# Optimization experiments

Hardware: AMD Instinct MI355X
Metric: run time of the kernel (lower is better)

Reference implementation:

```python
import jax, jax.numpy as jnp
import numpy as np

B, N, DM, S = 128, 1024, 64, 2
D_IN = 1 + 1 + 2 + DM  # x(1) + m(1) + u(2) + h(DM)


def setup_inputs() -> dict:
    key = jax.random.key(0)
    ks = jax.random.split(key, 12)
    return {
        "x": jax.random.normal(ks[0], (B, 1, N), jnp.float32),
        "m": jax.random.uniform(ks[1], (B, 1, N), jnp.float32),
        "u": jax.random.normal(ks[2], (B, 2, N), jnp.float32),
        "h": jax.random.normal(ks[3], (B, DM, N), jnp.float32),
        # stack of support_len row-normalized-ish adjacencies [S, N, N]
        "adj": jax.random.uniform(ks[4], (S, N, N), jnp.float32) / N,
        "W_in": jax.random.normal(ks[5], (DM, D_IN), jnp.float32) * 0.05,
        "b_in": jnp.zeros((DM,), jnp.float32),
        "W_gc": jax.random.normal(ks[6], (DM, S * DM), jnp.float32) * 0.05,
        "b_gc": jnp.zeros((DM,), jnp.float32),
        "W_out": jax.random.normal(ks[7], (DM, 2 * DM), jnp.float32) * 0.05,
        "b_out": jnp.zeros((DM,), jnp.float32),
        "W_read": jax.random.normal(ks[8], (1, 2 * DM), jnp.float32) * 0.05,
        "b_read": jnp.zeros((1,), jnp.float32),
        "prelu_w": jnp.full((1,), 0.25, jnp.float32),
    }


def _conv1x1(x, W, b):
    # Conv1d(kernel_size=1): [b,c,n] x [o,c] -> [b,o,n]
    return jnp.einsum('bcn,oc->bon', x, W) + b[None, :, None]


def reference(x, m, u, h, adj, W_in, b_in, W_gc, b_gc, W_out, b_out, W_read, b_read, prelu_w):
    # concat inputs on channel dim, then 1x1 conv to d_model
    x_in = jnp.concatenate([x, m, u, h], axis=1)            # [b, d_in, n]
    x_in = _conv1x1(x_in, W_in, b_in)                        # [b, dm, n]
    # SpatialConvOrderK (order=1, include_self=False):
    # per-support aggregation einsum('ncvl,wv->ncwl') with l==1
    agg = jnp.einsum('bcv,swv->bscw', x_in, adj)             # [b, S, dm, n]
    b_, s_, c_, n_ = agg.shape
    agg = agg.reshape(b_, s_ * c_, n_)                       # support-major concat
    gc = _conv1x1(agg, W_gc, b_gc)                           # [b, dm, n]
    out = jnp.concatenate([gc, h], axis=1)                   # [b, 2dm, n]
    out = _conv1x1(out, W_out, b_out)
    out = jnp.where(out >= 0, out, prelu_w[0] * out)         # PReLU (1 param)
    out = jnp.concatenate([out, h], axis=1)                  # [b, 2dm, n]
    return _conv1x1(out, W_read, b_read), out
```

## Files before the change

kernel.cpp:

```cpp
#include <hip/hip_runtime.h>
#include <hip/hip_bf16.h>
#include <stdint.h>

#define NB 128
#define NN 1024
#define NDM 64

typedef __bf16 bf16;
typedef __bf16 bf16x8_t __attribute__((ext_vector_type(8)));
typedef __bf16 bf16x4_t __attribute__((ext_vector_type(4)));
typedef __bf16 bf16x2_t __attribute__((ext_vector_type(2)));
typedef float f32x4 __attribute__((ext_vector_type(4)));

__global__ __launch_bounds__(256) void k_prep_w(
    const float* __restrict__ W_in, const float* __restrict__ b_in,
    const float* __restrict__ W_gc, const float* __restrict__ b_gc,
    const float* __restrict__ W_out, const float* __restrict__ b_out,
    const float* __restrict__ W_read,
    bf16* __restrict__ WAT, float* __restrict__ WYX, float* __restrict__ BIAS,
    bf16* __restrict__ W1B) {
  int i = blockIdx.x * 256 + threadIdx.x;
  if (i < 13312) {
    int r = i >> 6, cc = i & 63;
    int cq = cc >> 3, j = cc & 7;
    int c = ((cq ^ (r & 7)) << 3) + j;
    float val;
    if (r < 128) {
      int s = r >> 6, o = r & 63;
      val = 0.f;
      for (int k = 0; k < 64; ++k) val += W_gc[o * 128 + s * 64 + k] * W_in[k * 68 + 4 + c];
    } else if (r < 192) {
      val = W_out[(r - 128) * 128 + 64 + c];
    } else if (r == 192) {
      val = W_read[64 + c];
    } else {
      val = 0.f;
    }
    WAT[i] = (bf16)val;
  } else if (i < 13824) {
    int idx = i - 13312;
    int r = idx >> 2, j = idx & 3;
    int s = r >> 6, o = r & 63;
    float val = 0.f;
    for (int k = 0; k < 64; ++k) val += W_gc[o * 128 + s * 64 + k] * W_in[k * 68 + j];
    WYX[idx] = val;
  } else if (i < 14032) {
    int r = i - 13824;
    float val = 0.f;
    if (r < 128) {
      int s = r >> 6, o = r & 63;
      for (int k = 0; k < 64; ++k) val += W_gc[o * 128 + s * 64 + k] * b_in[k];
    } else if (r < 192) {
      int o = r - 128;
      val = b_out[o];
      for (int k = 0; k < 64; ++k) val += W_out[o * 128 + k] * b_gc[k];
    }
    BIAS[r] = val;
  } else if (i < 18128) {
    int j = i - 14032;
    int o = j >> 6, c = j & 63;
    W1B[j] = (bf16)W_out[o * 128 + c];
  }
}

__global__ __launch_bounds__(256) void k_adj_bf16(
    const float* __restrict__ adj, bf16* __restrict__ adjb) {
  int i = blockIdx.x * 256 + threadIdx.x;
  float4 v = reinterpret_cast<const float4*>(adj)[i];
  bf16x4_t r;
  r.x = (bf16)v.x; r.y = (bf16)v.y; r.z = (bf16)v.z; r.w = (bf16)v.w;
  reinterpret_cast<bf16x4_t*>(adjb)[i] = r;
}

__global__ __launch_bounds__(256) void k_ht(
    const float* __restrict__ h, bf16* __restrict__ HT, float* __restrict__ out2) {
  __shared__ __align__(16) float T[64 * 128];
  const int t = threadIdx.x;
  const int vb = blockIdx.x * 128;
  const int b = blockIdx.y;
  for (int i = t; i < 2048; i += 256) {
    int r = i >> 5, ck = i & 31;
    float4 v4 = *reinterpret_cast<const float4*>(&h[(size_t)(b * 64 + r) * NN + vb + ck * 4]);
    *reinterpret_cast<float4*>(&T[r * 128 + ck * 4]) = v4;
    *reinterpret_cast<float4*>(&out2[(size_t)(b * 128 + 64 + r) * NN + vb + ck * 4]) = v4;
  }
  __syncthreads();
  const int v = t >> 1, half = t & 1;
#pragma unroll
  for (int cc = 0; cc < 4; ++cc) {
    int cq = half * 4 + cc;
    int cbase = (cq ^ (v & 7)) << 3;
    bf16x8_t pk;
#pragma unroll
    for (int j = 0; j < 8; ++j) pk[j] = (bf16)T[(cbase + j) * 128 + v];
    *reinterpret_cast<bf16x8_t*>(&HT[((size_t)b * NN + vb + v) * 64 + cq * 8]) = pk;
  }
}

__global__ __launch_bounds__(256) void k_build_y(
    const float* __restrict__ x, const float* __restrict__ m, const float* __restrict__ u,
    const bf16* __restrict__ HT, const bf16* __restrict__ WAT,
    const float* __restrict__ WYX, const float* __restrict__ BIAS,
    bf16* __restrict__ Y, float* __restrict__ out2, float* __restrict__ hread) {
  __shared__ __align__(16) bf16 HTs[128 * 64];
  __shared__ __align__(16) bf16 WAs[208 * 64];
  __shared__ __align__(16) float X4L[128 * 4];
  __shared__ __align__(16) float WYXs[128 * 4];
  __shared__ __align__(16) float biasL[208];
  const int t = threadIdx.x;
  const int vb = blockIdx.x * 128;
  const int b = blockIdx.y;

  {
    const bf16* src = HT + ((size_t)b * NN + vb) * 64;
    for (int i = t; i < 1024; i += 256)
      __builtin_amdgcn_global_load_lds((const uint32_t*)(src + i * 8), (uint32_t*)&HTs[i * 8], 16, 0, 0);
    for (int i = t; i < 1664; i += 256)
      __builtin_amdgcn_global_load_lds((const uint32_t*)(WAT + i * 8), (uint32_t*)&WAs[i * 8], 16, 0, 0);
    if (t < 128)
      __builtin_amdgcn_global_load_lds((const uint32_t*)(WYX + t * 4), (uint32_t*)&WYXs[t * 4], 16, 0, 0);
    if (t < 52)
      __builtin_amdgcn_global_load_lds((const uint32_t*)(BIAS + t * 4), (uint32_t*)&biasL[t * 4], 16, 0, 0);
    if (t < 128) {
      int v = t;
      float4 x4;
      x4.x = x[(size_t)b * NN + vb + v];
      x4.y = m[(size_t)b * NN + vb + v];
      x4.z = u[(size_t)(b * 2) * NN + vb + v];
      x4.w = u[(size_t)(b * 2 + 1) * NN + vb + v];
      *reinterpret_cast<float4*>(&X4L[v * 4]) = x4;
    }
  }
  __syncthreads();

  const int wave = t >> 6, lane = t & 63;
  const int q = lane >> 4, lx = lane & 7, o16 = lane & 15;

#pragma unroll
  for (int vi = 0; vi < 2; ++vi) {
    const int vt = wave + vi * 4;
    const int vrow = vt * 16 + o16;
    bf16x8_t af0 = *reinterpret_cast<const bf16x8_t*>(&HTs[vrow * 64 + ((q ^ lx) << 3)]);
    bf16x8_t af1 = *reinterpret_cast<const bf16x8_t*>(&HTs[vrow * 64 + (((q + 4) ^ lx) << 3)]);
    float4 x4r[4];
#pragma unroll
    for (int r = 0; r < 4; ++r)
      x4r[r] = *reinterpret_cast<const float4*>(&X4L[(vt * 16 + q * 4 + r) * 4]);
    const int vg = vb + vt * 16 + q * 4;
    for (int nt = 0; nt < 13; ++nt) {
      const int rr = nt * 16 + o16;
      bf16x8_t bf0 = *reinterpret_cast<const bf16x8_t*>(&WAs[rr * 64 + ((q ^ lx) << 3)]);
      bf16x8_t bf1 = *reinterpret_cast<const bf16x8_t*>(&WAs[rr * 64 + (((q + 4) ^ lx) << 3)]);
      float bsv = biasL[rr];
      f32x4 c0 = {bsv, bsv, bsv, bsv};
      if (nt < 8) {
        float4 wy = *reinterpret_cast<const float4*>(&WYXs[rr * 4]);
#pragma unroll
        for (int r = 0; r < 4; ++r)
          c0[r] += wy.x * x4r[r].x + wy.y * x4r[r].y + wy.z * x4r[r].z + wy.w * x4r[r].w;
      }
      f32x4 acc = __builtin_amdgcn_mfma_f32_16x16x32_bf16(af0, bf0, c0, 0, 0, 0);
      acc = __builtin_amdgcn_mfma_f32_16x16x32_bf16(af1, bf1, acc, 0, 0, 0);
      if (nt < 8) {
        const int s = nt >> 2;
        const int o = rr - s * 64;
        bf16x4_t pk;
        pk.x = (bf16)acc[0]; pk.y = (bf16)acc[1]; pk.z = (bf16)acc[2]; pk.w = (bf16)acc[3];
        *reinterpret_cast<bf16x4_t*>(&Y[(size_t)(b * 64 + o) * 2048 + s * 1024 + vg]) = pk;
      } else if (nt < 12) {
        const int o = rr - 128;
        float4 st; st.x = acc[0]; st.y = acc[1]; st.z = acc[2]; st.w = acc[3];
        *reinterpret_cast<float4*>(&out2[(size_t)(b * 128 + o) * NN + vg]) = st;
      } else if (o16 == 0) {
        float4 st; st.x = acc[0]; st.y = acc[1]; st.z = acc[2]; st.w = acc[3];
        *reinterpret_cast<float4*>(&hread[(size_t)b * NN + vg]) = st;
      }
    }
  }
}

__global__ __launch_bounds__(256) void k_gemm(
    const bf16* __restrict__ Y, const bf16* __restrict__ ADJB,
    const bf16* __restrict__ W1B, const float* __restrict__ W_read,
    const float* __restrict__ b_read, const float* __restrict__ prelu_w,
    const float* __restrict__ hread, float* __restrict__ out0, float* __restrict__ out2) {
  __shared__ __align__(16) union SMem {
    struct { bf16 As[128 * 64]; bf16 Bs[128 * 64]; } st;
    bf16 gcs[2 * 128 * 72];
  } sm;
  __shared__ __align__(16) bf16 W1s[64 * 72];
  __shared__ float Wrs[64];

  const int t = threadIdx.x;
  const int wave = t >> 6, lane = t & 63;
  const int rowA = blockIdx.x * 128;
  const int colB = blockIdx.y * 128;
  const int wm = (wave & 1) * 64, wn = (wave >> 1) * 64;
  const int fr = lane & 15;
  const int q  = lane >> 4;

  for (int i = t; i < 4096; i += 256) W1s[(i >> 6) * 72 + (i & 63)] = W1B[i];
  if (t < 64) Wrs[t] = W_read[t];
  const float pw = prelu_w[0];
  const float br = b_read[0];

  f32x4 acc[4][4];
  const f32x4 zero = {0.f, 0.f, 0.f, 0.f};
#pragma unroll
  for (int i = 0; i < 4; ++i)
#pragma unroll
    for (int j = 0; j < 4; ++j) acc[i][j] = zero;

  int srow[4], sq[4];
#pragma unroll
  for (int j = 0; j < 4; ++j) {
    int c = t + 256 * j;
    srow[j] = c >> 3;
    sq[j] = (c & 7) ^ (srow[j] & 7);
  }
  __syncthreads();

  for (int k0 = 0; k0 < 2048; k0 += 64) {
    const int s = k0 >> 10, v0 = k0 & 1023;
    const bf16* bbase = ADJB + (size_t)s * (1024 * 1024) + v0;
#pragma unroll
    for (int j = 0; j < 4; ++j) {
      int c = t + 256 * j;
      __builtin_amdgcn_global_load_lds(
          (const uint32_t*)(Y + (size_t)(rowA + srow[j]) * 2048 + k0 + sq[j] * 8),
          (uint32_t*)&sm.st.As[c * 8], 16, 0, 0);
    }
#pragma unroll
    for (int j = 0; j < 4; ++j) {
      int c = t + 256 * j;
      __builtin_amdgcn_global_load_lds(
          (const uint32_t*)(bbase + (size_t)(colB + srow[j]) * 1024 + sq[j] * 8),
          (uint32_t*)&sm.st.Bs[c * 8], 16, 0, 0);
    }
    __syncthreads();
#pragma unroll
    for (int k2 = 0; k2 < 64; k2 += 32) {
      bf16x8_t af[4], bfr[4];
#pragma unroll
      for (int i = 0; i < 4; ++i) {
        const int r = wm + i * 16 + fr;
        af[i] = *reinterpret_cast<const bf16x8_t*>(
            &sm.st.As[r * 64 + ((((k2 >> 3) + q) ^ (r & 7)) << 3)]);
      }
#pragma unroll
      for (int i = 0; i < 4; ++i) {
        const int r = wn + i * 16 + fr;
        bfr[i] = *reinterpret_cast<const bf16x8_t*>(
            &sm.st.Bs[r * 64 + ((((k2 >> 3) + q) ^ (r & 7)) << 3)]);
      }
#pragma unroll
      for (int i = 0; i < 4; ++i)
#pragma unroll
        for (int j = 0; j < 4; ++j)
          acc[i][j] = __builtin_amdgcn_mfma_f32_16x16x32_bf16(af[i], bfr[j], acc[i][j], 0, 0, 0);
    }
    __syncthreads();
  }

  {
    const int b2w = wm >> 6;
#pragma unroll
    for (int i = 0; i < 4; ++i) {
      const int cc0 = i * 16 + (lane >> 4) * 4;
#pragma unroll
      for (int j = 0; j < 4; ++j) {
        const int wl = wn + j * 16 + (lane & 15);
        bf16x4_t r;
        r.x = (bf16)acc[i][j][0]; r.y = (bf16)acc[i][j][1];
        r.z = (bf16)acc[i][j][2]; r.w = (bf16)acc[i][j][3];
        *reinterpret_cast<bf16x4_t*>(&sm.gcs[b2w * 9216 + wl * 72 + cc0]) = r;
      }
    }
  }
  __syncthreads();

  const int b2 = wave >> 1, jh = wave & 1;
  const int b = blockIdx.x * 2 + b2;
  const int fk = q * 8;

  f32x4 acc2[4][4];
#pragma unroll
  for (int i = 0; i < 4; ++i)
#pragma unroll
    for (int j = 0; j < 4; ++j) acc2[i][j] = zero;

#pragma unroll
  for (int k2 = 0; k2 < 64; k2 += 32) {
    bf16x8_t af2[4], bf2[4];
#pragma unroll
    for (int i = 0; i < 4; ++i)
      af2[i] = *reinterpret_cast<const bf16x8_t*>(&W1s[(i * 16 + fr) * 72 + k2 + fk]);
#pragma unroll
    for (int j = 0; j < 4; ++j)
      bf2[j] = *reinterpret_cast<const bf16x8_t*>(&sm.gcs[b2 * 9216 + (jh * 64 + j * 16 + fr) * 72 + k2 + fk]);
#pragma unroll
    for (int i = 0; i < 4; ++i)
#pragma unroll
      for (int j = 0; j < 4; ++j)
        acc2[i][j] = __builtin_amdgcn_mfma_f32_16x16x32_bf16(af2[i], bf2[j], acc2[i][j], 0, 0, 0);
  }

  float rd[4] = {0.f, 0.f, 0.f, 0.f};
#pragma unroll
  for (int i = 0; i < 4; ++i) {
    const int ob = i * 16 + (lane >> 4) * 4;
#pragma unroll
    for (int r = 0; r < 4; ++r) {
      const int o = ob + r;
      const float wr = Wrs[o];
#pragma unroll
      for (int j = 0; j < 4; ++j) {
        const int wg = colB + jh * 64 + j * 16 + (lane & 15);
        float* p = &out2[(size_t)(b * 128 + o) * 1024 + wg];
        float val = acc2[i][j][r] + *p;
        val = val >= 0.f ? val : pw * val;
        *p = val;
        rd[j] += wr * val;
      }
    }
  }
#pragma unroll
  for (int j = 0; j < 4; ++j) {
    rd[j] += __shfl_xor(rd[j], 16, 64);
    rd[j] += __shfl_xor(rd[j], 32, 64);
  }
  if (lane < 16) {
#pragma unroll
    for (int j = 0; j < 4; ++j) {
      const int wg = colB + jh * 64 + j * 16 + lane;
      out0[(size_t)b * 1024 + wg] = rd[j] + hread[(size_t)b * 1024 + wg] + br;
    }
  }
}

extern "C" void kernel_launch(void* const* d_in, const int* in_sizes, int n_in,
                              void* d_out, int out_size, void* d_ws, size_t ws_size,
                              hipStream_t stream) {
  (void)in_sizes; (void)n_in; (void)out_size; (void)ws_size;
  const float* x       = (const float*)d_in[0];
  const float* m       = (const float*)d_in[1];
  const float* u       = (const float*)d_in[2];
  const float* h       = (const float*)d_in[3];
  const float* adj     = (const float*)d_in[4];
  const float* W_in    = (const float*)d_in[5];
  const float* b_in    = (const float*)d_in[6];
  const float* W_gc    = (const float*)d_in[7];
  const float* b_gc    = (const float*)d_in[8];
  const float* W_out   = (const float*)d_in[9];
  const float* b_out   = (const float*)d_in[10];
  const float* W_read  = (const float*)d_in[11];
  const float* b_read  = (const float*)d_in[12];
  const float* prelu_w = (const float*)d_in[13];

  char* ws = (char*)d_ws;
  bf16*  Y     = (bf16*)(ws);
  bf16*  ADJB  = (bf16*)(ws + 33554432);
  bf16*  HT    = (bf16*)(ws + 37748736);
  float* HREAD = (float*)(ws + 54525952);
  bf16*  WAT   = (bf16*)(ws + 55050240);
  float* WYX   = (float*)(ws + 55076864);
  float* BIAS  = (float*)(ws + 55078912);
  bf16*  W1B   = (bf16*)(ws + 55079936);

  float* out0 = (float*)d_out;
  float* out2 = out0 + 131072;

  hipLaunchKernelGGL(k_prep_w,  dim3(71),        dim3(256), 0, stream,
                     W_in, b_in, W_gc, b_gc, W_out, b_out, W_read, WAT, WYX, BIAS, W1B);
  hipLaunchKernelGGL(k_adj_bf16,dim3(2048),      dim3(256), 0, stream, adj, ADJB);
  hipLaunchKernelGGL(k_ht,      dim3(8, 128),    dim3(256), 0, stream, h, HT, out2);
  hipLaunchKernelGGL(k_build_y, dim3(8, 128),    dim3(256), 0, stream,
                     x, m, u, HT, WAT, WYX, BIAS, Y, out2, HREAD);
  hipLaunchKernelGGL(k_gemm,    dim3(64, 8),     dim3(256), 0, stream,
                     Y, ADJB, W1B, W_read, b_read, prelu_w, HREAD, out0, out2);
}
```

Before: 201.0 us.

## Fuse prep kernels and move h-projection epilogue into GEMM

Merges the adjacency bf16 conversion with weight prep, and fuses the h transpose into the Y-building kernel so h is read once via direct-to-LDS loads. The W_out·h and W_read·h terms are no longer precomputed into out2/hread; the GEMM epilogue computes them with extra MFMAs reading HT. This removes a full fp32 write and read-modify-write of the out2 first half plus the hread buffer, in exchange for more epilogue MFMA work and uncached HT global loads in the GEMM.

Result: faster. 183.9 us (-8.5%).

```diff
diff --git a/kernel.cpp b/kernel.cpp
--- a/kernel.cpp
+++ b/kernel.cpp
@@ -9,186 +9,172 @@
 typedef __bf16 bf16;
 typedef __bf16 bf16x8_t __attribute__((ext_vector_type(8)));
 typedef __bf16 bf16x4_t __attribute__((ext_vector_type(4)));
-typedef __bf16 bf16x2_t __attribute__((ext_vector_type(2)));
 typedef float f32x4 __attribute__((ext_vector_type(4)));
 
-__global__ __launch_bounds__(256) void k_prep_w(
+__global__ __launch_bounds__(256) void k_prep(
+    const float* __restrict__ adj,
     const float* __restrict__ W_in, const float* __restrict__ b_in,
     const float* __restrict__ W_gc, const float* __restrict__ b_gc,
     const float* __restrict__ W_out, const float* __restrict__ b_out,
     const float* __restrict__ W_read,
-    bf16* __restrict__ WAT, float* __restrict__ WYX, float* __restrict__ BIAS,
-    bf16* __restrict__ W1B) {
-  int i = blockIdx.x * 256 + threadIdx.x;
-  if (i < 13312) {
+    bf16* __restrict__ adjb, bf16* __restrict__ WAT, float* __restrict__ WYX,
+    float* __restrict__ BIAS, bf16* __restrict__ W1B, bf16* __restrict__ A2B,
+    float* __restrict__ HBv) {
+  const int bx = blockIdx.x;
+  if (bx < 2048) {
+    int i = bx * 256 + threadIdx.x;
+    float4 v = reinterpret_cast<const float4*>(adj)[i];
+    bf16x4_t r;
+    r.x = (bf16)v.x; r.y = (bf16)v.y; r.z = (bf16)v.z; r.w = (bf16)v.w;
+    reinterpret_cast<bf16x4_t*>(adjb)[i] = r;
+    return;
+  }
+  int i = (bx - 2048) * 256 + threadIdx.x;
+  if (i < 8192) {
     int r = i >> 6, cc = i & 63;
     int cq = cc >> 3, j = cc & 7;
     int c = ((cq ^ (r & 7)) << 3) + j;
-    float val;
-    if (r < 128) {
-      int s = r >> 6, o = r & 63;
-      val = 0.f;
-      for (int k = 0; k < 64; ++k) val += W_gc[o * 128 + s * 64 + k] * W_in[k * 68 + 4 + c];
-    } else if (r < 192) {
-      val = W_out[(r - 128) * 128 + 64 + c];
-    } else if (r == 192) {
-      val = W_read[64 + c];
-    } else {
-      val = 0.f;
-    }
-    WAT[i] = (bf16)val;
-  } else if (i < 13824) {
-    int idx = i - 13312;
-    int r = idx >> 2, j = idx & 3;
     int s = r >> 6, o = r & 63;
     float val = 0.f;
-    for (int k = 0; k < 64; ++k) val += W_gc[o * 128 + s * 64 + k] * W_in[k * 68 + j];
+    for (int k = 0; k < 64; ++k) val += W_gc[o * 128 + s * 64 + k] * W_in[k * 68 + 4 + c];
+    WAT[i] = (bf16)val;
+  } else if (i < 8704) {
+    int idx = i - 8192;
+    int r = idx >> 2, jj = idx & 3;
+    int s = r >> 6, o = r & 63;
+    float val = 0.f;
+    for (int k = 0; k < 64; ++k) val += W_gc[o * 128 + s * 64 + k] * W_in[k * 68 + jj];
     WYX[idx] = val;
-  } else if (i < 14032) {
-    int r = i - 13824;
+  } else if (i < 8832) {
+    int r = i - 8704;
+    int s = r >> 6, o = r & 63;
     float val = 0.f;
-    if (r < 128) {
-      int s = r >> 6, o = r & 63;
-      for (int k = 0; k < 64; ++k) val += W_gc[o * 128 + s * 64 + k] * b_in[k];
-    } else if (r < 192) {
-      int o = r - 128;
-      val = b_out[o];
-      for (int k = 0; k < 64; ++k) val += W_out[o * 128 + k] * b_gc[k];
-    }
+    for (int k = 0; k < 64; ++k) val += W_gc[o * 128 + s * 64 + k] * b_in[k];
     BIAS[r] = val;
-  } else if (i < 18128) {
-    int j = i - 14032;
+  } else if (i < 12928) {
+    int j = i - 8832;
     int o = j >> 6, c = j & 63;
     W1B[j] = (bf16)W_out[o * 128 + c];
+  } else if (i < 18048) {
+    int j = i - 12928;
+    int r = j >> 6, c = j & 63;
+    float val = 0.f;
+    if (r < 64) val = W_out[r * 128 + 64 + c];
+    else if (r == 64) val = W_read[64 + c];
+    A2B[j] = (bf16)val;
+  } else if (i < 18112) {
+    int o = i - 18048;
+    float val = b_out[o];
+    for (int c = 0; c < 64; ++c) val += W_out[o * 128 + c] * b_gc[c];
+    HBv[o] = val;
   }
 }
 
-__global__ __launch_bounds__(256) void k_adj_bf16(
-    const float* __restrict__ adj, bf16* __restrict__ adjb) {
-  int i = blockIdx.x * 256 + threadIdx.x;
-  float4 v = reinterpret_cast<const float4*>(adj)[i];
-  bf16x4_t r;
-  r.x = (bf16)v.x; r.y = (bf16)v.y; r.z = (bf16)v.z; r.w = (bf16)v.w;
-  reinterpret_cast<bf16x4_t*>(adjb)[i] = r;
-}
-
-__global__ __launch_bounds__(256) void k_ht(
-    const float* __restrict__ h, bf16* __restrict__ HT, float* __restrict__ out2) {
+__global__ __launch_bounds__(256) void k_build(
+    const float* __restrict__ x, const float* __restrict__ m, const float* __restrict__ u,
+    const float* __restrict__ h, const bf16* __restrict__ WAT,
+    const float* __restrict__ WYX, const float* __restrict__ BIAS,
+    bf16* __restrict__ Y, bf16* __restrict__ HT, float* __restrict__ out2) {
   __shared__ __align__(16) float T[64 * 128];
+  __shared__ __align__(16) bf16 HTs[128 * 64];
+  __shared__ __align__(16) bf16 WAs[128 * 64];
+  __shared__ __align__(16) float X4L[128 * 4];
+  __shared__ __align__(16) float WYXs[128 * 4];
+  __shared__ __align__(16) float biasL[128];
   const int t = threadIdx.x;
   const int vb = blockIdx.x * 128;
   const int b = blockIdx.y;
+
+  for (int i = t; i < 2048; i += 256)
+    __builtin_amdgcn_global_load_lds(
+        (const uint32_t*)(h + (size_t)(b * 64 + (i >> 5)) * NN + vb + (i & 31) * 4),
+        (uint32_t*)&T[i * 4], 16, 0, 0);
+  for (int i = t; i < 1024; i += 256)
+    __builtin_amdgcn_global_load_lds((const uint32_t*)(WAT + i * 8), (uint32_t*)&WAs[i * 8], 16, 0, 0);
+  if (t < 128)
+    __builtin_amdgcn_global_load_lds((const uint32_t*)(WYX + t * 4), (uint32_t*)&WYXs[t * 4], 16, 0, 0);
+  if (t < 32)
+    __builtin_amdgcn_global_load_lds((const uint32_t*)(BIAS + t * 4), (uint32_t*)&biasL[t * 4], 16, 0, 0);
+  if (t < 128) {
+    float4 x4;
+    x4.x = x[(size_t)b * NN + vb + t];
+    x4.y = m[(size_t)b * NN + vb + t];
+    x4.z = u[(size_t)(b * 2) * NN + vb + t];
+    x4.w = u[(size_t)(b * 2 + 1) * NN + vb + t];
+    *reinterpret_cast<float4*>(&X4L[t * 4]) = x4;
+  }
+  __syncthreads();
+
+  {
+    const int v = t >> 1, half = t & 1;
+#pragma unroll
+    for (int cc = 0; cc < 4; ++cc) {
+      int cq = half * 4 + cc;
+      int cbase = (cq ^ (v & 7)) << 3;
+      bf16x8_t pk;
+#pragma unroll
+      for (int j = 0; j < 8; ++j) pk[j] = (bf16)T[(cbase + j) * 128 + v];
+      *reinterpret_cast<bf16x8_t*>(&HTs[v * 64 + cq * 8]) = pk;
+      *reinterpret_cast<bf16x8_t*>(&HT[((size_t)(b << 10) + vb + v) * 64 + cq * 8]) = pk;
+    }
+  }
   for (int i = t; i < 2048; i += 256) {
     int r = i >> 5, ck = i & 31;
-    float4 v4 = *reinterpret_cast<const float4*>(&h[(size_t)(b * 64 + r) * NN + vb + ck * 4]);
-    *reinterpret_cast<float4*>(&T[r * 128 + ck * 4]) = v4;
-    *reinterpret_cast<float4*>(&out2[(size_t)(b * 128 + 64 + r) * NN + vb + ck * 4]) = v4;
-  }
-  __syncthreads();
-  const int v = t >> 1, half = t & 1;
-#pragma unroll
-  for (int cc = 0; cc < 4; ++cc) {
-    int cq = half * 4 + cc;
-    int cbase = (cq ^ (v & 7)) << 3;
-    bf16x8_t pk;
-#pragma unroll
-    for (int j = 0; j < 8; ++j) pk[j] = (bf16)T[(cbase + j) * 128 + v];
-    *reinterpret_cast<bf16x8_t*>(&HT[((size_t)b * NN + vb + v) * 64 + cq * 8]) = pk;
-  }
-}
-
-__global__ __launch_bounds__(256) void k_build_y(
-    const float* __restrict__ x, const float* __restrict__ m, const float* __restrict__ u,
-    const bf16* __restrict__ HT, const bf16* __restrict__ WAT,
-    const float* __restrict__ WYX, const float* __restrict__ BIAS,
-    bf16* __restrict__ Y, float* __restrict__ out2, float* __restrict__ hread) {
-  __shared__ __align__(16) bf16 HTs[128 * 64];
-  __shared__ __align__(16) bf16 WAs[208 * 64];
-  __shared__ __align__(16) float X4L[128 * 4];
-  __shared__ __align__(16) float WYXs[128 * 4];
-  __shared__ __align__(16) float biasL[208];
-  const int t = threadIdx.x;
-  const int vb = blockIdx.x * 128;
-  const int b = blockIdx.y;
-
-  {
-    const bf16* src = HT + ((size_t)b * NN + vb) * 64;
-    for (int i = t; i < 1024; i += 256)
-      __builtin_amdgcn_global_load_lds((const uint32_t*)(src + i * 8), (uint32_t*)&HTs[i * 8], 16, 0, 0);
-    for (int i = t; i < 1664; i += 256)
-      __builtin_amdgcn_global_load_lds((const uint32_t*)(WAT + i * 8), (uint32_t*)&WAs[i * 8], 16, 0, 0);
-    if (t < 128)
-      __builtin_amdgcn_global_load_lds((const uint32_t*)(WYX + t * 4), (uint32_t*)&WYXs[t * 4], 16, 0, 0);
-    if (t < 52)
-      __builtin_amdgcn_global_load_lds((const uint32_t*)(BIAS + t * 4), (uint32_t*)&biasL[t * 4], 16, 0, 0);
-    if (t < 128) {
-      int v = t;
-      float4 x4;
-      x4.x = x[(size_t)b * NN + vb + v];
-      x4.y = m[(size_t)b * NN + vb + v];
-      x4.z = u[(size_t)(b * 2) * NN + vb + v];
-      x4.w = u[(size_t)(b * 2 + 1) * NN + vb + v];
-      *reinterpret_cast<float4*>(&X4L[v * 4]) = x4;
-    }
+    float4 hv = *reinterpret_cast<const float4*>(&T[r * 128 + ck * 4]);
+    *reinterpret_cast<float4*>(&out2[(size_t)(b * 128 + 64 + r) * NN + vb + ck * 4]) = hv;
   }
   __syncthreads();
 
   const int wave = t >> 6, lane = t & 63;
   const int q = lane >> 4, lx = lane & 7, o16 = lane & 15;
+  const int offK0 = (q ^ lx) << 3, offK1 = ((q + 4) ^ lx) << 3;
 
 #pragma unroll
   for (int vi = 0; vi < 2; ++vi) {
     const int vt = wave + vi * 4;
     const int vrow = vt * 16 + o16;
-    bf16x8_t af0 = *reinterpret_cast<const bf16x8_t*>(&HTs[vrow * 64 + ((q ^ lx) << 3)]);
-    bf16x8_t af1 = *reinterpret_cast<const bf16x8_t*>(&HTs[vrow * 64 + (((q + 4) ^ lx) << 3)]);
+    bf16x8_t af0 = *reinterpret_cast<const bf16x8_t*>(&HTs[vrow * 64 + offK0]);
+    bf16x8_t af1 = *reinterpret_cast<const bf16x8_t*>(&HTs[vrow * 64 + offK1]);
     float4 x4r[4];
 #pragma unroll
     for (int r = 0; r < 4; ++r)
       x4r[r] = *reinterpret_cast<const float4*>(&X4L[(vt * 16 + q * 4 + r) * 4]);
     const int vg = vb + vt * 16 + q * 4;
-    for (int nt = 0; nt < 13; ++nt) {
+    for (int nt = 0; nt < 8; ++nt) {
       const int rr = nt * 16 + o16;
-      bf16x8_t bf0 = *reinterpret_cast<const bf16x8_t*>(&WAs[rr * 64 + ((q ^ lx) << 3)]);
-      bf16x8_t bf1 = *reinterpret_cast<const bf16x8_t*>(&WAs[rr * 64 + (((q + 4) ^ lx) << 3)]);
+      bf16x8_t bf0 = *reinterpret_cast<const bf16x8_t*>(&WAs[rr * 64 + offK0]);
+      bf16x8_t bf1 = *reinterpret_cast<const bf16x8_t*>(&WAs[rr * 64 + offK1]);
       float bsv = biasL[rr];
-      f32x4 c0 = {bsv, bsv, bsv, bsv};
-      if (nt < 8) {
-        float4 wy = *reinterpret_cast<const float4*>(&WYXs[rr * 4]);
-#pragma unroll
-        for (int r = 0; r < 4; ++r)
-          c0[r] += wy.x * x4r[r].x + wy.y * x4r[r].y + wy.z * x4r[r].z + wy.w * x4r[r].w;
-      }
+      float4 wy = *reinterpret_cast<const float4*>(&WYXs[rr * 4]);
+      f32x4 c0;
+#pragma unroll
+      for (int r = 0; r < 4; ++r)
+        c0[r] = bsv + wy.x * x4r[r].x + wy.y * x4r[r].y + wy.z * x4r[r].z + wy.w * x4r[r].w;
       f32x4 acc = __builtin_amdgcn_mfma_f32_16x16x32_bf16(af0, bf0, c0, 0, 0, 0);
       acc = __builtin_amdgcn_mfma_f32_16x16x32_bf16(af1, bf1, acc, 0, 0, 0);
-      if (nt < 8) {
-        const int s = nt >> 2;
-        const int o = rr - s * 64;
-        bf16x4_t pk;
-        pk.x = (bf16)acc[0]; pk.y = (bf16)acc[1]; pk.z = (bf16)acc[2]; pk.w = (bf16)acc[3];
-        *reinterpret_cast<bf16x4_t*>(&Y[(size_t)(b * 64 + o) * 2048 + s * 1024 + vg]) = pk;
-      } else if (nt < 12) {
-        const int o = rr - 128;
-        float4 st; st.x = acc[0]; st.y = acc[1]; st.z = acc[2]; st.w = acc[3];
-        *reinterpret_cast<float4*>(&out2[(size_t)(b * 128 + o) * NN + vg]) = st;
-      } else if (o16 == 0) {
-        float4 st; st.x = acc[0]; st.y = acc[1]; st.z = acc[2]; st.w = acc[3];
-        *reinterpret_cast<float4*>(&hread[(size_t)b * NN + vg]) = st;
-      }
+      const int s = nt >> 2;
+      const int o = rr - s * 64;
+      bf16x4_t pk;
+      pk.x = (bf16)acc[0]; pk.y = (bf16)acc[1]; pk.z = (bf16)acc[2]; pk.w = (bf16)acc[3];
+      *reinterpret_cast<bf16x4_t*>(&Y[(size_t)(b * 64 + o) * 2048 + s * 1024 + vg]) = pk;
     }
   }
 }
 
 __global__ __launch_bounds__(256) void k_gemm(
     const bf16* __restrict__ Y, const bf16* __restrict__ ADJB,
-    const bf16* __restrict__ W1B, const float* __restrict__ W_read,
+    const bf16* __restrict__ HT,
+    const bf16* __restrict__ W1B, const bf16* __restrict__ A2B,
+    const float* __restrict__ HBv, const float* __restrict__ W_read,
     const float* __restrict__ b_read, const float* __restrict__ prelu_w,
-    const float* __restrict__ hread, float* __restrict__ out0, float* __restrict__ out2) {
+    float* __restrict__ out0, float* __restrict__ out2) {
   __shared__ __align__(16) union SMem {
     struct { bf16 As[128 * 64]; bf16 Bs[128 * 64]; } st;
     bf16 gcs[2 * 128 * 72];
   } sm;
   __shared__ __align__(16) bf16 W1s[64 * 72];
+  __shared__ __align__(16) bf16 A2s[80 * 72];
+  __shared__ float HBs[64];
   __shared__ float Wrs[64];
 
   const int t = threadIdx.x;
@@ -197,10 +183,12 @@
   const int colB = blockIdx.y * 128;
   const int wm = (wave & 1) * 64, wn = (wave >> 1) * 64;
   const int fr = lane & 15;
-  const int q  = lane >> 4;
+  const int q = lane >> 4, lx = lane & 7;
+  const int offK0 = (q ^ lx) << 3, offK1 = ((q + 4) ^ lx) << 3;
 
   for (int i = t; i < 4096; i += 256) W1s[(i >> 6) * 72 + (i & 63)] = W1B[i];
-  if (t < 64) Wrs[t] = W_read[t];
+  for (int i = t; i < 5120; i += 256) A2s[(i >> 6) * 72 + (i & 63)] = A2B[i];
+  if (t < 64) { HBs[t] = HBv[t]; Wrs[t] = W_read[t]; }
   const float pw = prelu_w[0];
   const float br = b_read[0];
 
@@ -211,65 +199,71 @@
 #pragma unroll
     for (int j = 0; j < 4; ++j) acc[i][j] = zero;
 
-  int srow[4], sq[4];
+  const bf16* aSrc[4]; const bf16* bSrc[4];
+  uint32_t* aDst[4]; uint32_t* bDst[4];
 #pragma unroll
   for (int j = 0; j < 4; ++j) {
     int c = t + 256 * j;
-    srow[j] = c >> 3;
-    sq[j] = (c & 7) ^ (srow[j] & 7);
+    int row = c >> 3;
+    int qs = (c & 7) ^ (row & 7);
+    aSrc[j] = Y + (size_t)(rowA + row) * 2048 + qs * 8;
+    bSrc[j] = ADJB + (size_t)(colB + row) * 1024 + qs * 8;
+    aDst[j] = (uint32_t*)&sm.st.As[c * 8];
+    bDst[j] = (uint32_t*)&sm.st.Bs[c * 8];
+  }
+  int rAb[4], rBb[4];
+#pragma unroll
+  for (int i = 0; i < 4; ++i) {
+    rAb[i] = (wm + i * 16 + fr) * 64;
+    rBb[i] = (wn + i * 16 + fr) * 64;
   }
   __syncthreads();
 
-  for (int k0 = 0; k0 < 2048; k0 += 64) {
-    const int s = k0 >> 10, v0 = k0 & 1023;
-    const bf16* bbase = ADJB + (size_t)s * (1024 * 1024) + v0;
-#pragma unroll
-    for (int j = 0; j < 4; ++j) {
-      int c = t + 256 * j;
-      __builtin_amdgcn_global_load_lds(
-          (const uint32_t*)(Y + (size_t)(rowA + srow[j]) * 2048 + k0 + sq[j] * 8),
-          (uint32_t*)&sm.st.As[c * 8], 16, 0, 0);
-    }
-#pragma unroll
-    for (int j = 0; j < 4; ++j) {
-      int c = t + 256 * j;
-      __builtin_amdgcn_global_load_lds(
-          (const uint32_t*)(bbase + (size_t)(colB + srow[j]) * 1024 + sq[j] * 8),
-          (uint32_t*)&sm.st.Bs[c * 8], 16, 0, 0);
-    }
-    __syncthreads();
-#pragma unroll
-    for (int k2 = 0; k2 < 64; k2 += 32) {
-      bf16x8_t af[4], bfr[4];
-#pragma unroll
-      for (int i = 0; i < 4; ++i) {
-        const int r = wm + i * 16 + fr;
-        af[i] = *reinterpret_cast<const bf16x8_t*>(
-            &sm.st.As[r * 64 + ((((k2 >> 3) + q) ^ (r & 7)) << 3)]);
-      }
-#pragma unroll
-      for (int i = 0; i < 4; ++i) {
-        const int r = wn + i * 16 + fr;
-        bfr[i] = *reinterpret_cast<const bf16x8_t*>(
-            &sm.st.Bs[r * 64 + ((((k2 >> 3) + q) ^ (r & 7)) << 3)]);
-      }
-#pragma unroll
-      for (int i = 0; i < 4; ++i)
-#pragma unroll
-        for (int j = 0; j < 4; ++j)
-          acc[i][j] = __builtin_amdgcn_mfma_f32_16x16x32_bf16(af[i], bfr[j], acc[i][j], 0, 0, 0);
-    }
-    __syncthreads();
+  for (int s = 0; s < 2; ++s) {
+    for (int kk = 0; kk < 1024; kk += 64) {
+#pragma unroll
+      for (int j = 0; j < 4; ++j) {
+        __builtin_amdgcn_global_load_lds((const uint32_t*)aSrc[j], aDst[j], 16, 0, 0);
+        aSrc[j] += 64;
+      }
+#pragma unroll
+      for (int j = 0; j < 4; ++j) {
+        __builtin_amdgcn_global_load_lds((const uint32_t*)bSrc[j], bDst[j], 16, 0, 0);
+        bSrc[j] += 64;
+      }
+      __syncthreads();
+#pragma unroll
+      for (int k2 = 0; k2 < 2; ++k2) {
+        const int off = k2 ? offK1 : offK0;
+        bf16x8_t af[4], bfr[4];
+#pragma unroll
+        for (int i = 0; i < 4; ++i)
+          af[i] = *reinterpret_cast<const bf16x8_t*>(&sm.st.As[rAb[i] + off]);
+#pragma unroll
+        for (int i = 0; i < 4; ++i)
+          bfr[i] = *reinterpret_cast<const bf16x8_t*>(&sm.st.Bs[rBb[i] + off]);
+#pragma unroll
+        for (int i = 0; i < 4; ++i)
+#pragma unroll
+          for (int j = 0; j < 4; ++j)
+            acc[i][j] = __builtin_amdgcn_mfma_f32_16x16x32_bf16(af[i], bfr[j], acc[i][j], 0, 0, 0);
+      }
+      __syncthreads();
+    }
+    if (s == 0) {
+#pragma unroll
+      for (int j = 0; j < 4; ++j) bSrc[j] += (1024 * 1024 - 1024);
+    }
   }
 
   {
     const int b2w = wm >> 6;
 #pragma unroll
     for (int i = 0; i < 4; ++i) {
-      const int cc0 = i * 16 + (lane >> 4) * 4;
+      const int cc0 = i * 16 + q * 4;
 #pragma unroll
       for (int j = 0; j < 4; ++j) {
-        const int wl = wn + j * 16 + (lane & 15);
+        const int wl = wn + j * 16 + fr;
         bf16x4_t r;
         r.x = (bf16)acc[i][j][0]; r.y = (bf16)acc[i][j][1];
         r.z = (bf16)acc[i][j][2]; r.w = (bf16)acc[i][j][3];
@@ -281,23 +275,31 @@
 
   const int b2 = wave >> 1, jh = wave & 1;
   const int b = blockIdx.x * 2 + b2;
-  const int fk = q * 8;
-
-  f32x4 acc2[4][4];
-#pragma unroll
-  for (int i = 0; i < 4; ++i)
-#pragma unroll
-    for (int j = 0; j < 4; ++j) acc2[i][j] = zero;
+
+  f32x4 acc2[5][4];
+#pragma unroll
+  for (int i = 0; i < 5; ++i)
+#pragma unroll
+    for (int j = 0; j < 4; ++j) {
+      if (i < 4) {
+        f32x4 c0;
+#pragma unroll
+        for (int r = 0; r < 4; ++r) c0[r] = HBs[i * 16 + q * 4 + r];
+        acc2[i][j] = c0;
+      } else {
+        acc2[i][j] = zero;
+      }
+    }
 
 #pragma unroll
   for (int k2 = 0; k2 < 64; k2 += 32) {
     bf16x8_t af2[4], bf2[4];
 #pragma unroll
     for (int i = 0; i < 4; ++i)
-      af2[i] = *reinterpret_cast<const bf16x8_t*>(&W1s[(i * 16 + fr) * 72 + k2 + fk]);
+      af2[i] = *reinterpret_cast<const bf16x8_t*>(&W1s[(i * 16 + fr) * 72 + k2 + q * 8]);
 #pragma unroll
     for (int j = 0; j < 4; ++j)
-      bf2[j] = *reinterpret_cast<const bf16x8_t*>(&sm.gcs[b2 * 9216 + (jh * 64 + j * 16 + fr) * 72 + k2 + fk]);
+      bf2[j] = *reinterpret_cast<const bf16x8_t*>(&sm.gcs[b2 * 9216 + (jh * 64 + j * 16 + fr) * 72 + k2 + q * 8]);
 #pragma unroll
     for (int i = 0; i < 4; ++i)
 #pragma unroll
@@ -305,21 +307,38 @@
         acc2[i][j] = __builtin_amdgcn_mfma_f32_16x16x32_bf16(af2[i], bf2[j], acc2[i][j], 0, 0, 0);
   }
 
+#pragma unroll
+  for (int k2 = 0; k2 < 64; k2 += 32) {
+    const int off = k2 ? offK1 : offK0;
+    bf16x8_t bh[4], af3[5];
+#pragma unroll
+    for (int j = 0; j < 4; ++j) {
+      const int w = colB + jh * 64 + j * 16 + fr;
+      bh[j] = *reinterpret_cast<const bf16x8_t*>(&HT[((size_t)(b << 10) + w) * 64 + off]);
+    }
+#pragma unroll
+    for (int i = 0; i < 5; ++i)
+      af3[i] = *reinterpret_cast<const bf16x8_t*>(&A2s[(i * 16 + fr) * 72 + k2 + q * 8]);
+#pragma unroll
+    for (int i = 0; i < 5; ++i)
+#pragma unroll
+      for (int j = 0; j < 4; ++j)
+        acc2[i][j] = __builtin_amdgcn_mfma_f32_16x16x32_bf16(af3[i], bh[j], acc2[i][j], 0, 0, 0);
+  }
+
   float rd[4] = {0.f, 0.f, 0.f, 0.f};
 #pragma unroll
   for (int i = 0; i < 4; ++i) {
-    const int ob = i * 16 + (lane >> 4) * 4;
 #pragma unroll
     for (int r = 0; r < 4; ++r) {
-      const int o = ob + r;
+      const int o = i * 16 + q * 4 + r;
       const float wr = Wrs[o];
 #pragma unroll
       for (int j = 0; j < 4; ++j) {
-        const int wg = colB + jh * 64 + j * 16 + (lane & 15);
-        float* p = &out2[(size_t)(b * 128 + o) * 1024 + wg];
-        float val = acc2[i][j][r] + *p;
+        const int wg = colB + jh * 64 + j * 16 + fr;
+        float val = acc2[i][j][r];
         val = val >= 0.f ? val : pw * val;
-        *p = val;
+        out2[(size_t)(b * 128 + o) * 1024 + wg] = val;
         rd[j] += wr * val;
       }
     }
@@ -333,7 +352,7 @@
 #pragma unroll
     for (int j = 0; j < 4; ++j) {
       const int wg = colB + jh * 64 + j * 16 + lane;
-      out0[(size_t)b * 1024 + wg] = rd[j] + hread[(size_t)b * 1024 + wg] + br;
+      out0[(size_t)b * 1024 + wg] = rd[j] + acc2[4][j][0] + br;
     }
   }
 }
@@ -358,24 +377,24 @@
   const float* prelu_w = (const float*)d_in[13];
 
   char* ws = (char*)d_ws;
-  bf16*  Y     = (bf16*)(ws);
-  bf16*  ADJB  = (bf16*)(ws + 33554432);
-  bf16*  HT    = (bf16*)(ws + 37748736);
-  float* HREAD = (float*)(ws + 54525952);
-  bf16*  WAT   = (bf16*)(ws + 55050240);
-  float* WYX   = (float*)(ws + 55076864);
-  float* BIAS  = (float*)(ws + 55078912);
-  bf16*  W1B   = (bf16*)(ws + 55079936);
+  bf16*  Y    = (bf16*)(ws);
+  bf16*  ADJB = (bf16*)(ws + 33554432);
+  bf16*  HT   = (bf16*)(ws + 37748736);
+  bf16*  WAT  = (bf16*)(ws + 54525952);
+  float* WYX  = (float*)(ws + 54542336);
+  float* BIAS = (float*)(ws + 54544384);
+  bf16*  W1B  = (bf16*)(ws + 54544896);
+  bf16*  A2B  = (bf16*)(ws + 54553088);
+  float* HBv  = (float*)(ws + 54563328);
 
   float* out0 = (float*)d_out;
   float* out2 = out0 + 131072;
 
-  hipLaunchKernelGGL(k_prep_w,  dim3(71),        dim3(256), 0, stream,
-                     W_in, b_in, W_gc, b_gc, W_out, b_out, W_read, WAT, WYX, BIAS, W1B);
-  hipLaunchKernelGGL(k_adj_bf16,dim3(2048),      dim3(256), 0, stream, adj, ADJB);
-  hipLaunchKernelGGL(k_ht,      dim3(8, 128),    dim3(256), 0, stream, h, HT, out2);
-  hipLaunchKernelGGL(k_build_y, dim3(8, 128),    dim3(256), 0, stream,
-                     x, m, u, HT, WAT, WYX, BIAS, Y, out2, HREAD);
-  hipLaunchKernelGGL(k_gemm,    dim3(64, 8),     dim3(256), 0, stream,
-                     Y, ADJB, W1B, W_read, b_read, prelu_w, HREAD, out0, out2);
+  hipLaunchKernelGGL(k_prep,  dim3(2119),     dim3(256), 0, stream,
+                     adj, W_in, b_in, W_gc, b_gc, W_out, b_out, W_read,
+                     ADJB, WAT, WYX, BIAS, W1B, A2B, HBv);
+  hipLaunchKernelGGL(k_build, dim3(8, 128),   dim3(256), 0, stream,
+                     x, m, u, h, WAT, WYX, BIAS, Y, HT, out2);
+  hipLaunchKernelGGL(k_gemm,  dim3(64, 8),    dim3(256), 0, stream,
+                     Y, ADJB, HT, W1B, A2B, HBv, W_read, b_read, prelu_w, out0, out2);
 }
```
